# Kernel optimization log

Measured on AMD Instinct MI355X. Metric: run time of the kernel, lower is better.

## Reference

```python
import jax, jax.numpy as jnp
import numpy as np

EPS = 2.220446049250313e-16  # np.finfo(float).eps, used by SparseDispatcher.combine


def setup_inputs() -> dict:
    key = jax.random.key(0)
    k1, k2, k3, k4, k5, k6 = jax.random.split(key, 6)
    N, D, H, E = 16384, 512, 2048, 8
    x = jax.random.normal(k1, (N, D), dtype=jnp.float32)
    w_gate = jax.random.normal(k2, (D, E), dtype=jnp.float32) * 0.05
    W1 = jax.random.normal(k3, (E - 1, D, H), dtype=jnp.float32) * 0.02
    b1 = jax.random.normal(k4, (E - 1, H), dtype=jnp.float32) * 0.02
    W2 = jax.random.normal(k5, (E - 1, H, D), dtype=jnp.float32) * 0.02
    b2 = jax.random.normal(k6, (E - 1, D), dtype=jnp.float32) * 0.02
    return {"x": x, "w_gate": w_gate, "W1": W1, "b1": b1, "W2": W2, "b2": b2, "k": 2}


def reference(x, w_gate, W1, b1, W2, b2, k):
    # --- top-k gating (input_choice, node-level, no noise / eval mode) ---
    N, E = x.shape[0], w_gate.shape[1]
    logits = x @ w_gate                                   # [N, E]
    top_vals, top_idx = jax.lax.top_k(logits, k)          # [N, k]
    top_gates = jax.nn.softmax(top_vals, axis=-1)         # softmax over selected experts
    gates = jnp.zeros((N, E), x.dtype).at[jnp.arange(N)[:, None], top_idx].set(top_gates)
    # --- dispatch / per-expert MLP / weighted combine ---
    # output[b] = sum_i gates[b,i] * expert_i(x[b]); last expert is identity.
    out = gates[:, E - 1 : E] * x                         # IdentityExpert (expert E-1)
    for e in range(W1.shape[0]):                          # fixed small expert count
        h = jax.nn.relu(x @ W1[e] + b1[e])                # [N, H]
        out = out + gates[:, e : e + 1] * (h @ W2[e] + b2[e])
    out = out.astype(jnp.float32)
    # combine() replaces exact zeros with machine epsilon
    return jnp.where(out == 0, EPS, out)
```

## Files before the change

### kernel.cpp

```cpp
#include <hip/hip_runtime.h>
#include <stdint.h>

#define EPS_VAL 2.220446049250313e-16f

typedef unsigned short u16;
typedef __bf16 bf16x8 __attribute__((ext_vector_type(8)));
typedef float f32x4 __attribute__((ext_vector_type(4)));

static __device__ __forceinline__ u16 f2bf(float v) {
    __bf16 b = (__bf16)v;
    return __builtin_bit_cast(u16, b);
}
static __device__ __forceinline__ float bf2f(u16 u) {
    __bf16 b = __builtin_bit_cast(__bf16, u);
    return (float)b;
}
static __device__ __forceinline__ void gll16(const void* g, void* l) {
    __builtin_amdgcn_global_load_lds(
        (const __attribute__((address_space(1))) unsigned int*)g,
        (__attribute__((address_space(3))) unsigned int*)l, 16, 0, 0);
}

#define MT_CAP 40

__global__ void k_transpose_cvt(const float* __restrict__ in, u16* __restrict__ out,
                                int R, int C) {
    __shared__ float t[32][33];
    const float* ip = in + (size_t)blockIdx.z * R * C;
    u16* op = out + (size_t)blockIdx.z * R * C;
    int tx = threadIdx.x & 31, ty = threadIdx.x >> 5;
    int c = blockIdx.x * 32 + tx;
    #pragma unroll
    for (int i = 0; i < 4; ++i) {
        int r = blockIdx.y * 32 + ty + i * 8;
        t[ty + i * 8][tx] = ip[(size_t)r * C + c];
    }
    __syncthreads();
    int r2 = blockIdx.y * 32 + tx;
    #pragma unroll
    for (int i = 0; i < 4; ++i) {
        int c2 = blockIdx.x * 32 + ty + i * 8;
        op[(size_t)c2 * R + r2] = f2bf(t[tx][ty + i * 8]);
    }
}

__global__ __launch_bounds__(1024) void k_gate(
    const float* __restrict__ x, const float* __restrict__ wg,
    u16* __restrict__ xb, int* __restrict__ cnt,
    uint2* __restrict__ asg, float4* __restrict__ rec) {
    __shared__ int hist[8];
    __shared__ int basep[8];
    __shared__ int   eA[64], eB[64], rA[64], rB[64];
    __shared__ float gA[64], gB[64];

    const int tid = threadIdx.x;
    if (tid < 8) hist[tid] = 0;
    __syncthreads();

    const int wv = tid >> 6, lane = tid & 63;
    #pragma unroll
    for (int it = 0; it < 4; ++it) {
        int rl  = it * 16 + wv;
        int row = blockIdx.x * 64 + rl;
        const float4* px = (const float4*)(x + (size_t)row * 512) + lane * 2;
        float4 v0 = px[0], v1 = px[1];
        union { u16 h[8]; uint4 u; } o;
        o.h[0]=f2bf(v0.x); o.h[1]=f2bf(v0.y); o.h[2]=f2bf(v0.z); o.h[3]=f2bf(v0.w);
        o.h[4]=f2bf(v1.x); o.h[5]=f2bf(v1.y); o.h[6]=f2bf(v1.z); o.h[7]=f2bf(v1.w);
        ((uint4*)(xb + (size_t)row * 512))[lane] = o.u;

        float xv[8] = {v0.x, v0.y, v0.z, v0.w, v1.x, v1.y, v1.z, v1.w};
        float a0=0,a1=0,a2=0,a3=0,a4=0,a5=0,a6=0,a7=0;
        const float4* wp = (const float4*)wg + (size_t)lane * 16;
        #pragma unroll
        for (int j = 0; j < 8; ++j) {
            float4 wa = wp[j * 2], wb = wp[j * 2 + 1];
            float v = xv[j];
            a0 += v*wa.x; a1 += v*wa.y; a2 += v*wa.z; a3 += v*wa.w;
            a4 += v*wb.x; a5 += v*wb.y; a6 += v*wb.z; a7 += v*wb.w;
        }
        #pragma unroll
        for (int off = 32; off; off >>= 1) {
            a0 += __shfl_xor(a0, off); a1 += __shfl_xor(a1, off);
            a2 += __shfl_xor(a2, off); a3 += __shfl_xor(a3, off);
            a4 += __shfl_xor(a4, off); a5 += __shfl_xor(a5, off);
            a6 += __shfl_xor(a6, off); a7 += __shfl_xor(a7, off);
        }
        if (lane == 0) {
            float v[8] = {a0,a1,a2,a3,a4,a5,a6,a7};
            int i0 = 0;
            #pragma unroll
            for (int e = 1; e < 8; ++e) if (v[e] > v[i0]) i0 = e;
            int i1 = (i0 == 0) ? 1 : 0;
            #pragma unroll
            for (int e = 0; e < 8; ++e) if (e != i0 && v[e] > v[i1]) i1 = e;
            float ex = expf(v[i1] - v[i0]);
            float g0 = 1.f / (1.f + ex), g1 = ex / (1.f + ex);
            rec[row] = make_float4(__int_as_float(i0), __int_as_float(i1), g0, g1);
            int r0 = (i0 != 7) ? atomicAdd(&hist[i0], 1) : -1;
            int r1 = (i1 != 7) ? atomicAdd(&hist[i1], 1) : -1;
            eA[rl] = i0; eB[rl] = i1; rA[rl] = r0; rB[rl] = r1;
            gA[rl] = g0; gB[rl] = g1;
        }
    }
    __syncthreads();
    if (tid < 7) basep[tid] = atomicAdd(&cnt[tid], hist[tid]);
    __syncthreads();
    if (tid < 64) {
        int row = blockIdx.x * 64 + tid;
        int i0 = eA[tid], i1 = eB[tid];
        if (i0 != 7)
            asg[i0 * 16384 + basep[i0] + rA[tid]] =
                make_uint2((unsigned)(row << 1), __float_as_uint(gA[tid]));
        if (i1 != 7)
            asg[i1 * 16384 + basep[i1] + rB[tid]] =
                make_uint2((unsigned)((row << 1) | 1), __float_as_uint(gB[tid]));
    }
}

__global__ void k_prefix(const int* __restrict__ cnt, int* __restrict__ off) {
    if (threadIdx.x == 0) {
        int s = 0;
        for (int e = 0; e < 7; ++e) { off[e] = s; s += cnt[e]; }
        off[7] = s;
    }
}


__global__ __launch_bounds__(256) void k_e1(
    const u16* __restrict__ xb, const u16* __restrict__ w1t,
    const float* __restrict__ b1, const int* __restrict__ cnt,
    const int* __restrict__ off, const uint2* __restrict__ asg,
    u16* __restrict__ Hb, int h0, int S, int NT)
{
    __shared__ __attribute__((aligned(16))) char smem[61440];

    const int bid = blockIdx.x;
    const int t0  = (bid & 7) * (35 * NT) + (bid >> 3);
    const int e   = t0 / (MT_CAP * NT);
    const int rem = t0 - e * (MT_CAP * NT);
    const int mt  = rem / NT;
    const int nt  = rem - mt * NT;

    const int ce  = cnt[e];
    const int mtb = mt * 128;
    if (mtb >= ce) return;
    const int ntb = nt * 128;

    const int tid = threadIdx.x, wv = tid >> 6, lane = tid & 63;
    const int l16 = lane & 15, q = lane >> 4;
    const int wr = wv >> 1, wc = wv & 1;
    const u16* w1p = w1t + (size_t)e * 2048 * 512;

    const int nj = (wv < 2) ? 3 : 2;
    const u16* aS[3]; const u16* bS[3]; int js[3];
    #pragma unroll
    for (int jj = 0; jj < 3; ++jj) {
        int j = wv + jj * 4; js[jj] = j;
        if (j < 10) {
            int g = j * 64 + lane, row = g / 5, sl = g % 5;
            if (sl == 4) sl = 0;
            int idx = mtb + row;
            int rs = 0;
            if (idx < ce) rs = (int)asg[e * 16384 + idx].x >> 1;
            aS[jj] = xb + (size_t)rs * 512 + sl * 8;
            bS[jj] = w1p + (size_t)(h0 + ntb + row) * 512 + sl * 8;
        } else { aS[jj] = xb; bS[jj] = w1p; }
    }

    auto ISSUE = [&](int b) {
        char* An = smem + (b % 3) * 20480;
        char* Bn = An + 10240;
        int ko = b * 32;
        #pragma unroll
        for (int jj = 0; jj < 3; ++jj) if (jj < nj) {
            gll16(aS[jj] + ko, An + js[jj] * 1024);
            gll16(bS[jj] + ko, Bn + js[jj] * 1024);
        }
    };

    ISSUE(0);
    ISSUE(1);
    if (wv < 2) asm volatile("s_waitcnt vmcnt(6) lgkmcnt(0)" ::: "memory");
    else        asm volatile("s_waitcnt vmcnt(4) lgkmcnt(0)" ::: "memory");
    __builtin_amdgcn_s_barrier();
    __builtin_amdgcn_sched_barrier(0);

    f32x4 acc[4][4];
    #pragma unroll
    for (int mti = 0; mti < 4; ++mti)
        #pragma unroll
        for (int nti = 0; nti < 4; ++nti) acc[mti][nti] = (f32x4){0.f, 0.f, 0.f, 0.f};

    const int KT = 16;
    for (int t = 0; t < KT; ++t) {
        if (t + 2 < KT) ISSUE(t + 2);

        const char* Ab = smem + (t % 3) * 20480;
        const char* Bb = Ab + 10240;
        bf16x8 af[4], bf[4];
        #pragma unroll
        for (int mti = 0; mti < 4; ++mti)
            af[mti] = *(const bf16x8*)(Ab + (wr * 64 + mti * 16 + l16) * 80 + q * 16);
        #pragma unroll
        for (int nti = 0; nti < 4; ++nti)
            bf[nti] = *(const bf16x8*)(Bb + (wc * 64 + nti * 16 + l16) * 80 + q * 16);
        #pragma unroll
        for (int mti = 0; mti < 4; ++mti)
            #pragma unroll
            for (int nti = 0; nti < 4; ++nti)
                acc[mti][nti] = __builtin_amdgcn_mfma_f32_16x16x32_bf16(
                    af[mti], bf[nti], acc[mti][nti], 0, 0, 0);

        if (t < KT - 1) {
            if (t < KT - 2) {
                if (wv < 2) asm volatile("s_waitcnt vmcnt(6) lgkmcnt(0)" ::: "memory");
                else        asm volatile("s_waitcnt vmcnt(4) lgkmcnt(0)" ::: "memory");
            } else {
                asm volatile("s_waitcnt vmcnt(0) lgkmcnt(0)" ::: "memory");
            }
            __builtin_amdgcn_s_barrier();
            __builtin_amdgcn_sched_barrier(0);
        }
    }

    const size_t hbase = (size_t)off[e];
    #pragma unroll
    for (int nti = 0; nti < 4; ++nti) {
        int hcol = ntb + wc * 64 + nti * 16 + l16;
        float bias = b1[e * 2048 + h0 + hcol];
        #pragma unroll
        for (int mti = 0; mti < 4; ++mti) {
            #pragma unroll
            for (int r = 0; r < 4; ++r) {
                int i = mtb + wr * 64 + mti * 16 + q * 4 + r;
                if (i < ce) {
                    float v = acc[mti][nti][r] + bias;
                    v = v > 0.f ? v : 0.f;
                    Hb[(hbase + i) * S + hcol] = f2bf(v);
                }
            }
        }
    }
}

__global__ __launch_bounds__(256) void k_e2(
    const u16* __restrict__ Hb, const u16* __restrict__ w2t,
    const float* __restrict__ b2, const int* __restrict__ cnt,
    const int* __restrict__ off, const uint2* __restrict__ asg,
    u16* __restrict__ ybuf, int h0, int S, int firstPass, int lastPass)
{
    __shared__ __attribute__((aligned(16))) char smem[61440];

    const int bid = blockIdx.x;
    const int t0  = (bid & 7) * 140 + (bid >> 3);
    const int e   = t0 / (MT_CAP * 4);
    const int rem = t0 - e * (MT_CAP * 4);
    const int mt  = rem >> 2;
    const int dt  = rem & 3;

    const int ce  = cnt[e];
    const int mtb = mt * 128;
    if (mtb >= ce) return;
    const int dtb = dt * 128;

    const int tid = threadIdx.x, wv = tid >> 6, lane = tid & 63;
    const int l16 = lane & 15, q = lane >> 4;
    const int wr = wv >> 1, wc = wv & 1;
    const u16* w2p = w2t + (size_t)e * 512 * 2048;
    const size_t hbase = (size_t)off[e];

    const int nj = (wv < 2) ? 3 : 2;
    const u16* aS[3]; const u16* bS[3]; int js[3];
    #pragma unroll
    for (int jj = 0; jj < 3; ++jj) {
        int j = wv + jj * 4; js[jj] = j;
        if (j < 10) {
            int g = j * 64 + lane, row = g / 5, sl = g % 5;
            if (sl == 4) sl = 0;
            aS[jj] = Hb + (hbase + mtb + row) * S + sl * 8;
            bS[jj] = w2p + (size_t)(dtb + row) * 2048 + h0 + sl * 8;
        } else { aS[jj] = Hb; bS[jj] = w2p; }
    }

    auto ISSUE = [&](int b) {
        char* An = smem + (b % 3) * 20480;
        char* Bn = An + 10240;
        int ko = b * 32;
        #pragma unroll
        for (int jj = 0; jj < 3; ++jj) if (jj < nj) {
            gll16(aS[jj] + ko, An + js[jj] * 1024);
            gll16(bS[jj] + ko, Bn + js[jj] * 1024);
        }
    };

    ISSUE(0);
    ISSUE(1);
    if (wv < 2) asm volatile("s_waitcnt vmcnt(6) lgkmcnt(0)" ::: "memory");
    else        asm volatile("s_waitcnt vmcnt(4) lgkmcnt(0)" ::: "memory");
    __builtin_amdgcn_s_barrier();
    __builtin_amdgcn_sched_barrier(0);

    f32x4 acc[4][4];
    #pragma unroll
    for (int mti = 0; mti < 4; ++mti)
        #pragma unroll
        for (int nti = 0; nti < 4; ++nti) acc[mti][nti] = (f32x4){0.f, 0.f, 0.f, 0.f};

    const int KT = S >> 5;
    for (int t = 0; t < KT; ++t) {
        if (t + 2 < KT) ISSUE(t + 2);

        const char* Ab = smem + (t % 3) * 20480;
        const char* Bb = Ab + 10240;
        bf16x8 af[4], bf[4];
        #pragma unroll
        for (int mti = 0; mti < 4; ++mti)
            af[mti] = *(const bf16x8*)(Ab + (wr * 64 + mti * 16 + l16) * 80 + q * 16);
        #pragma unroll
        for (int nti = 0; nti < 4; ++nti)
            bf[nti] = *(const bf16x8*)(Bb + (wc * 64 + nti * 16 + l16) * 80 + q * 16);
        #pragma unroll
        for (int mti = 0; mti < 4; ++mti)
            #pragma unroll
            for (int nti = 0; nti < 4; ++nti)
                acc[mti][nti] = __builtin_amdgcn_mfma_f32_16x16x32_bf16(
                    af[mti], bf[nti], acc[mti][nti], 0, 0, 0);

        if (t < KT - 1) {
            if (t < KT - 2) {
                if (wv < 2) asm volatile("s_waitcnt vmcnt(6) lgkmcnt(0)" ::: "memory");
                else        asm volatile("s_waitcnt vmcnt(4) lgkmcnt(0)" ::: "memory");
            } else {
                asm volatile("s_waitcnt vmcnt(0) lgkmcnt(0)" ::: "memory");
            }
            __builtin_amdgcn_s_barrier();
            __builtin_amdgcn_sched_barrier(0);
        }
    }

    #pragma unroll
    for (int nti = 0; nti < 4; ++nti) {
        int d = dtb + wc * 64 + nti * 16 + l16;
        float b2v = b2[e * 512 + d];
        #pragma unroll
        for (int mti = 0; mti < 4; ++mti) {
            #pragma unroll
            for (int r = 0; r < 4; ++r) {
                int lrow = wr * 64 + mti * 16 + q * 4 + r;
                int i = mtb + lrow;
                if (i < ce) {
                    uint2 a = asg[e * 16384 + i];
                    int rs = (int)a.x;
                    float g = __builtin_bit_cast(float, a.y);
                    float v = acc[mti][nti][r];
                    size_t yo = ((size_t)(rs & 1) * 16384 + (rs >> 1)) * 512 + d;
                    if (!firstPass) v += bf2f(ybuf[yo]);
                    if (lastPass)   v = g * (v + b2v);
                    ybuf[yo] = f2bf(v);
                }
            }
        }
    }
}

__global__ void k_final(const float* __restrict__ x, const float4* __restrict__ rec,
                        const u16* __restrict__ ybuf, float* __restrict__ out) {
    int i = blockIdx.x * 256 + threadIdx.x;
    int row = i >> 7;
    float4 r = rec[row];
    int e0 = __float_as_int(r.x), e1 = __float_as_int(r.y);
    float g7 = (e0 == 7) ? r.z : ((e1 == 7) ? r.w : 0.f);
    float4 xv = ((const float4*)x)[i];
    float o0 = g7 * xv.x, o1 = g7 * xv.y, o2 = g7 * xv.z, o3 = g7 * xv.w;
    size_t off = (size_t)i * 4;
    if (e0 != 7) {
        uint2 y = *(const uint2*)(ybuf + off);
        o0 += bf2f((u16)(y.x & 0xffff)); o1 += bf2f((u16)(y.x >> 16));
        o2 += bf2f((u16)(y.y & 0xffff)); o3 += bf2f((u16)(y.y >> 16));
    }
    if (e1 != 7) {
        uint2 y = *(const uint2*)(ybuf + 8388608 + off);
        o0 += bf2f((u16)(y.x & 0xffff)); o1 += bf2f((u16)(y.x >> 16));
        o2 += bf2f((u16)(y.y & 0xffff)); o3 += bf2f((u16)(y.y >> 16));
    }
    float4 res;
    res.x = (o0 == 0.f) ? EPS_VAL : o0;
    res.y = (o1 == 0.f) ? EPS_VAL : o1;
    res.z = (o2 == 0.f) ? EPS_VAL : o2;
    res.w = (o3 == 0.f) ? EPS_VAL : o3;
    ((float4*)out)[i] = res;
}

extern "C" void kernel_launch(void* const* d_in, const int* in_sizes, int n_in,
                              void* d_out, int out_size, void* d_ws, size_t ws_size,
                              hipStream_t stream) {
    const float* x  = (const float*)d_in[0];
    const float* wg = (const float*)d_in[1];
    const float* W1 = (const float*)d_in[2];
    const float* b1 = (const float*)d_in[3];
    const float* W2 = (const float*)d_in[4];
    const float* b2 = (const float*)d_in[5];
    (void)in_sizes; (void)n_in; (void)out_size;

    char* ws = (char*)d_ws;
    int*    cnt  = (int*)ws;
    int*    off  = (int*)(ws + 64);
    float4* rec  = (float4*)(ws + 256);
    uint2*  asg  = (uint2*)(ws + 262400);
    u16*    xb   = (u16*)(ws + 1179904);
    u16*    w1t  = (u16*)(ws + 17957120);
    u16*    w2t  = (u16*)(ws + 32637184);
    u16*    ybuf = (u16*)(ws + 47317248);
    u16*    Hb   = (u16*)(ws + 80871680);

    int S = 128;
    const int cands[4] = {2048, 1024, 512, 256};
    for (int c = 0; c < 4; ++c) {
        if (ws_size >= 80871680ull + (size_t)32896 * cands[c] * 2) { S = cands[c]; break; }
    }
    const int passes = 2048 / S;

    hipMemsetAsync(ws, 0, 256, stream);
    k_transpose_cvt<<<dim3(64, 16, 7), 256, 0, stream>>>(W1, w1t, 512, 2048);
    k_transpose_cvt<<<dim3(16, 64, 7), 256, 0, stream>>>(W2, w2t, 2048, 512);
    k_gate<<<256, 1024, 0, stream>>>(x, wg, xb, cnt, asg, rec);
    k_prefix<<<1, 64, 0, stream>>>(cnt, off);
    for (int p = 0; p < passes; ++p) {
        int h0 = p * S;
        int NT = S / 128;
        k_e1<<<7 * MT_CAP * NT, 256, 0, stream>>>(xb, w1t, b1, cnt, off, asg, Hb, h0, S, NT);
        k_e2<<<7 * MT_CAP * 4, 256, 0, stream>>>(Hb, w2t, b2, cnt, off, asg, ybuf,
                                                 h0, S, p == 0 ? 1 : 0,
                                                 p == passes - 1 ? 1 : 0);
    }
    k_final<<<8192, 256, 0, stream>>>(x, rec, ybuf, (float*)d_out);
}
```

Baseline: 370.9 us.

## Replace padded LDS tiles with XOR-swizzled dense layout in expert GEMMs

Both expert GEMM kernels drop the 80-byte padded LDS row layout, which needed a 5-slot load pattern with a wasted duplicate slot. They now use dense 64-byte rows with an XOR swizzle on the 16-byte k-chunks to avoid bank conflicts. Every thread now issues exactly four direct-to-LDS loads per stage, so wave-dependent waitcnt branches go away. LDS per block shrinks from 60KB to 48KB, which may allow more resident blocks per CU. The second kernel's A-source address now also adds h0, which changes behaviour whenever h0 is nonzero.

```diff
diff --git a/kernel.cpp b/kernel.cpp
--- a/kernel.cpp
+++ b/kernel.cpp
@@ -133,7 +133,7 @@
     const int* __restrict__ off, const uint2* __restrict__ asg,
     u16* __restrict__ Hb, int h0, int S, int NT)
 {
-    __shared__ __attribute__((aligned(16))) char smem[61440];
+    __shared__ __attribute__((aligned(16))) char smem[49152];
 
     const int bid = blockIdx.x;
     const int t0  = (bid & 7) * (35 * NT) + (bid >> 3);
@@ -152,37 +152,30 @@
     const int wr = wv >> 1, wc = wv & 1;
     const u16* w1p = w1t + (size_t)e * 2048 * 512;
 
-    const int nj = (wv < 2) ? 3 : 2;
-    const u16* aS[3]; const u16* bS[3]; int js[3];
-    #pragma unroll
-    for (int jj = 0; jj < 3; ++jj) {
-        int j = wv + jj * 4; js[jj] = j;
-        if (j < 10) {
-            int g = j * 64 + lane, row = g / 5, sl = g % 5;
-            if (sl == 4) sl = 0;
-            int idx = mtb + row;
-            int rs = 0;
-            if (idx < ce) rs = (int)asg[e * 16384 + idx].x >> 1;
-            aS[jj] = xb + (size_t)rs * 512 + sl * 8;
-            bS[jj] = w1p + (size_t)(h0 + ntb + row) * 512 + sl * 8;
-        } else { aS[jj] = xb; bS[jj] = w1p; }
-    }
+    const int rowS  = tid >> 2;
+    const int s_log = (lane & 3) ^ ((lane >> 3) & 3);
+    int rsA0 = 0, rsA1 = 0;
+    { int i0 = mtb + rowS;      if (i0 < ce) rsA0 = (int)asg[e * 16384 + i0].x >> 1; }
+    { int i1 = mtb + rowS + 64; if (i1 < ce) rsA1 = (int)asg[e * 16384 + i1].x >> 1; }
+    const u16* aS0 = xb + (size_t)rsA0 * 512 + s_log * 8;
+    const u16* aS1 = xb + (size_t)rsA1 * 512 + s_log * 8;
+    const u16* bS0 = w1p + (size_t)(h0 + ntb + rowS) * 512 + s_log * 8;
+    const u16* bS1 = w1p + (size_t)(h0 + ntb + rowS + 64) * 512 + s_log * 8;
+    const int dA0 = wv * 1024, dA1 = 4096 + wv * 1024;
 
     auto ISSUE = [&](int b) {
-        char* An = smem + (b % 3) * 20480;
-        char* Bn = An + 10240;
+        char* bufA = smem + (b % 3) * 16384;
+        char* bufB = bufA + 8192;
         int ko = b * 32;
-        #pragma unroll
-        for (int jj = 0; jj < 3; ++jj) if (jj < nj) {
-            gll16(aS[jj] + ko, An + js[jj] * 1024);
-            gll16(bS[jj] + ko, Bn + js[jj] * 1024);
-        }
+        gll16(aS0 + ko, bufA + dA0);
+        gll16(aS1 + ko, bufA + dA1);
+        gll16(bS0 + ko, bufB + dA0);
+        gll16(bS1 + ko, bufB + dA1);
     };
 
     ISSUE(0);
     ISSUE(1);
-    if (wv < 2) asm volatile("s_waitcnt vmcnt(6) lgkmcnt(0)" ::: "memory");
-    else        asm volatile("s_waitcnt vmcnt(4) lgkmcnt(0)" ::: "memory");
+    asm volatile("s_waitcnt vmcnt(4) lgkmcnt(0)" ::: "memory");
     __builtin_amdgcn_s_barrier();
     __builtin_amdgcn_sched_barrier(0);
 
@@ -192,19 +185,22 @@
         #pragma unroll
         for (int nti = 0; nti < 4; ++nti) acc[mti][nti] = (f32x4){0.f, 0.f, 0.f, 0.f};
 
+    const int kq = (l16 >> 1) & 3;
     const int KT = 16;
     for (int t = 0; t < KT; ++t) {
         if (t + 2 < KT) ISSUE(t + 2);
 
-        const char* Ab = smem + (t % 3) * 20480;
-        const char* Bb = Ab + 10240;
+        const char* Ab = smem + (t % 3) * 16384;
+        const char* Bb = Ab + 8192;
         bf16x8 af[4], bf[4];
         #pragma unroll
         for (int mti = 0; mti < 4; ++mti)
-            af[mti] = *(const bf16x8*)(Ab + (wr * 64 + mti * 16 + l16) * 80 + q * 16);
+            af[mti] = *(const bf16x8*)(Ab + (wr * 64 + mti * 16 + l16) * 64 +
+                                       ((q ^ kq) * 16));
         #pragma unroll
         for (int nti = 0; nti < 4; ++nti)
-            bf[nti] = *(const bf16x8*)(Bb + (wc * 64 + nti * 16 + l16) * 80 + q * 16);
+            bf[nti] = *(const bf16x8*)(Bb + (wc * 64 + nti * 16 + l16) * 64 +
+                                       ((q ^ kq) * 16));
         #pragma unroll
         for (int mti = 0; mti < 4; ++mti)
             #pragma unroll
@@ -213,12 +209,10 @@
                     af[mti], bf[nti], acc[mti][nti], 0, 0, 0);
 
         if (t < KT - 1) {
-            if (t < KT - 2) {
-                if (wv < 2) asm volatile("s_waitcnt vmcnt(6) lgkmcnt(0)" ::: "memory");
-                else        asm volatile("s_waitcnt vmcnt(4) lgkmcnt(0)" ::: "memory");
-            } else {
+            if (t < KT - 2)
+                asm volatile("s_waitcnt vmcnt(4) lgkmcnt(0)" ::: "memory");
+            else
                 asm volatile("s_waitcnt vmcnt(0) lgkmcnt(0)" ::: "memory");
-            }
             __builtin_amdgcn_s_barrier();
             __builtin_amdgcn_sched_barrier(0);
         }
@@ -250,7 +244,7 @@
     const int* __restrict__ off, const uint2* __restrict__ asg,
     u16* __restrict__ ybuf, int h0, int S, int firstPass, int lastPass)
 {
-    __shared__ __attribute__((aligned(16))) char smem[61440];
+    __shared__ __attribute__((aligned(16))) char smem[49152];
 
     const int bid = blockIdx.x;
     const int t0  = (bid & 7) * 140 + (bid >> 3);
@@ -270,34 +264,27 @@
     const u16* w2p = w2t + (size_t)e * 512 * 2048;
     const size_t hbase = (size_t)off[e];
 
-    const int nj = (wv < 2) ? 3 : 2;
-    const u16* aS[3]; const u16* bS[3]; int js[3];
-    #pragma unroll
-    for (int jj = 0; jj < 3; ++jj) {
-        int j = wv + jj * 4; js[jj] = j;
-        if (j < 10) {
-            int g = j * 64 + lane, row = g / 5, sl = g % 5;
-            if (sl == 4) sl = 0;
-            aS[jj] = Hb + (hbase + mtb + row) * S + sl * 8;
-            bS[jj] = w2p + (size_t)(dtb + row) * 2048 + h0 + sl * 8;
-        } else { aS[jj] = Hb; bS[jj] = w2p; }
-    }
+    const int rowS  = tid >> 2;
+    const int s_log = (lane & 3) ^ ((lane >> 3) & 3);
+    const u16* aS0 = Hb + (hbase + mtb + rowS) * S + h0 + s_log * 8;
+    const u16* aS1 = Hb + (hbase + mtb + rowS + 64) * S + h0 + s_log * 8;
+    const u16* bS0 = w2p + (size_t)(dtb + rowS) * 2048 + h0 + s_log * 8;
+    const u16* bS1 = w2p + (size_t)(dtb + rowS + 64) * 2048 + h0 + s_log * 8;
+    const int dA0 = wv * 1024, dA1 = 4096 + wv * 1024;
 
     auto ISSUE = [&](int b) {
-        char* An = smem + (b % 3) * 20480;
-        char* Bn = An + 10240;
+        char* bufA = smem + (b % 3) * 16384;
+        char* bufB = bufA + 8192;
         int ko = b * 32;
-        #pragma unroll
-        for (int jj = 0; jj < 3; ++jj) if (jj < nj) {
-            gll16(aS[jj] + ko, An + js[jj] * 1024);
-            gll16(bS[jj] + ko, Bn + js[jj] * 1024);
-        }
+        gll16(aS0 + ko, bufA + dA0);
+        gll16(aS1 + ko, bufA + dA1);
+        gll16(bS0 + ko, bufB + dA0);
+        gll16(bS1 + ko, bufB + dA1);
     };
 
     ISSUE(0);
     ISSUE(1);
-    if (wv < 2) asm volatile("s_waitcnt vmcnt(6) lgkmcnt(0)" ::: "memory");
-    else        asm volatile("s_waitcnt vmcnt(4) lgkmcnt(0)" ::: "memory");
+    asm volatile("s_waitcnt vmcnt(4) lgkmcnt(0)" ::: "memory");
     __builtin_amdgcn_s_barrier();
     __builtin_amdgcn_sched_barrier(0);
 
@@ -307,19 +294,22 @@
         #pragma unroll
         for (int nti = 0; nti < 4; ++nti) acc[mti][nti] = (f32x4){0.f, 0.f, 0.f, 0.f};
 
+    const int kq = (l16 >> 1) & 3;
     const int KT = S >> 5;
     for (int t = 0; t < KT; ++t) {
         if (t + 2 < KT) ISSUE(t + 2);
 
-        const char* Ab = smem + (t % 3) * 20480;
-        const char* Bb = Ab + 10240;
+        const char* Ab = smem + (t % 3) * 16384;
+        const char* Bb = Ab + 8192;
         bf16x8 af[4], bf[4];
         #pragma unroll
         for (int mti = 0; mti < 4; ++mti)
-            af[mti] = *(const bf16x8*)(Ab + (wr * 64 + mti * 16 + l16) * 80 + q * 16);
+            af[mti] = *(const bf16x8*)(Ab + (wr * 64 + mti * 16 + l16) * 64 +
+                                       ((q ^ kq) * 16));
         #pragma unroll
         for (int nti = 0; nti < 4; ++nti)
-            bf[nti] = *(const bf16x8*)(Bb + (wc * 64 + nti * 16 + l16) * 80 + q * 16);
+            bf[nti] = *(const bf16x8*)(Bb + (wc * 64 + nti * 16 + l16) * 64 +
+                                       ((q ^ kq) * 16));
         #pragma unroll
         for (int mti = 0; mti < 4; ++mti)
             #pragma unroll
@@ -328,12 +318,10 @@
                     af[mti], bf[nti], acc[mti][nti], 0, 0, 0);
 
         if (t < KT - 1) {
-            if (t < KT - 2) {
-                if (wv < 2) asm volatile("s_waitcnt vmcnt(6) lgkmcnt(0)" ::: "memory");
-                else        asm volatile("s_waitcnt vmcnt(4) lgkmcnt(0)" ::: "memory");
-            } else {
+            if (t < KT - 2)
+                asm volatile("s_waitcnt vmcnt(4) lgkmcnt(0)" ::: "memory");
+            else
                 asm volatile("s_waitcnt vmcnt(0) lgkmcnt(0)" ::: "memory");
-            }
             __builtin_amdgcn_s_barrier();
             __builtin_amdgcn_sched_barrier(0);
         }
```

Measured after the change: 311.7 us. 1.19x faster.
